# Performance work log

Hardware: AMD Instinct MI355X
Metric: run time of the kernel (lower is better)

## Reference

```python
import jax, jax.numpy as jnp
import numpy as np

# Binary (sign) weight linear: y = x @ sign(W)^T + b

def _binarize(w):
    # sign with sign(0) mapped to +1, as in typical BinaryLinear impls
    return jnp.where(w >= 0, 1.0, -1.0).astype(w.dtype)

def setup_inputs() -> dict:
    key = jax.random.key(0)
    ks = jax.random.split(key, 7)
    B = 65536
    x = jax.random.normal(ks[0], (B, 28, 28), dtype=jnp.float32)
    W1 = jax.random.normal(ks[1], (1000, 784), dtype=jnp.float32) * 0.05
    b1 = jax.random.normal(ks[2], (1000,), dtype=jnp.float32) * 0.01
    W2 = jax.random.normal(ks[3], (500, 1000), dtype=jnp.float32) * 0.05
    b2 = jax.random.normal(ks[4], (500,), dtype=jnp.float32) * 0.01
    W3 = jax.random.normal(ks[5], (10, 500), dtype=jnp.float32) * 0.05
    b3 = jax.random.normal(ks[6], (10,), dtype=jnp.float32) * 0.01
    return {"x": x, "W1": W1, "b1": b1, "W2": W2, "b2": b2, "W3": W3, "b3": b3}

def reference(x, W1, b1, W2, b2, W3, b3):
    h = x.reshape(x.shape[0], -1)                      # [B, 784]
    h = jnp.maximum(h @ _binarize(W1).T + b1, 0.0)     # [B, 1000]
    h = jnp.maximum(h @ _binarize(W2).T + b2, 0.0)     # [B, 500]
    return h @ _binarize(W3).T + b3                    # [B, 10]
```

## Files before the change

kernel.cpp:

```cpp
#include <hip/hip_runtime.h>
#include <stdint.h>


typedef __attribute__((ext_vector_type(8))) short bf16x8;
typedef __attribute__((ext_vector_type(4))) float f32x4;

typedef const __attribute__((address_space(1))) unsigned int* as1_u32p;
typedef __attribute__((address_space(3))) unsigned int* as3_u32p;

__device__ __forceinline__ void glds16(const void* g, void* l) {
  __builtin_amdgcn_global_load_lds((as1_u32p)g, (as3_u32p)l, 16, 0, 0);
}

__device__ __forceinline__ unsigned short f2bf(float f) {
  union { float f; unsigned u; } c;
  c.f = f;
  unsigned u = c.u;
  u += 0x7FFFu + ((u >> 16) & 1u);
  return (unsigned short)(u >> 16);
}

__global__ void binarize_kernel(const float* __restrict__ src, int Ns, int Ks,
                                short* __restrict__ dst, int Np, int Kp) {
  int idx = blockIdx.x * 256 + threadIdx.x;
  if (idx >= Np * Kp) return;
  int n = idx / Kp;
  int k = idx - n * Kp;
  short v = 0;
  if (n < Ns && k < Ks)
    v = (src[n * Ks + k] >= 0.0f) ? (short)0x3F80 : (short)0xBF80;
  dst[idx] = v;
}

__global__ __launch_bounds__(256, 2)
void gemm1_kernel(const float* __restrict__ X, const short* __restrict__ Wb,
                  const float* __restrict__ bias, short* __restrict__ H) {
  constexpr int K = 784, KP = 800, NP = 1024, NR = 1000;
  __shared__ short As[128 * 32];
  __shared__ short Bs[128 * 32];

  const int d = blockIdx.x;
  const int xcd = d & 7;
  const int j = d >> 3;
  const int m0 = ((xcd << 6) + (j >> 3)) * 128;
  const int n0 = (j & 7) * 128;

  const int tid = threadIdx.x;
  const int lane = tid & 63;
  const int wave = tid >> 6;
  const int wm = wave >> 1, wn = wave & 1;
  const int l15 = lane & 15;
  const int quad = lane >> 4;

  const int ar = tid >> 1;
  const int aks = (tid & 1) * 16;
  const float* xrow = X + (size_t)(m0 + ar) * K;
  short* adst = As + ar * 32 + aks;

  const int br = wave * 16 + (lane >> 2);
  const int bks = (lane & 3) * 8;
  const short* brow0 = Wb + (size_t)(n0 + br) * KP + bks;
  short* bdst = Bs + (wave * 16) * 32;

  f32x4 acc[4][4];
#pragma unroll
  for (int i = 0; i < 4; ++i)
#pragma unroll
    for (int j2 = 0; j2 < 4; ++j2) acc[i][j2] = (f32x4){0.f, 0.f, 0.f, 0.f};

  for (int k0 = 0; k0 < KP; k0 += 32) {
    glds16(brow0 + k0, bdst);
    glds16(brow0 + k0 + (size_t)64 * KP, bdst + 64 * 32);
    short tmp[16];
#pragma unroll
    for (int c = 0; c < 4; ++c) {
      const int kk = k0 + aks + c * 4;
      float4 f;
      if (kk < K)
        f = *(const float4*)(xrow + kk);
      else
        f = make_float4(0.f, 0.f, 0.f, 0.f);
      tmp[c * 4 + 0] = (short)f2bf(f.x);
      tmp[c * 4 + 1] = (short)f2bf(f.y);
      tmp[c * 4 + 2] = (short)f2bf(f.z);
      tmp[c * 4 + 3] = (short)f2bf(f.w);
    }
    *(bf16x8*)(adst) = *(bf16x8*)(tmp);
    *(bf16x8*)(adst + 8) = *(bf16x8*)(tmp + 8);

    __syncthreads();

    const short* abase = As + (size_t)(wm * 64 + l15) * 32 + quad * 8;
    const short* bbase = Bs + (size_t)(wn * 64 + l15) * 32 + quad * 8;
    bf16x8 af[4], bfr[4];
#pragma unroll
    for (int i = 0; i < 4; ++i) af[i] = *(const bf16x8*)(abase + i * 16 * 32);
#pragma unroll
    for (int j2 = 0; j2 < 4; ++j2) bfr[j2] = *(const bf16x8*)(bbase + j2 * 16 * 32);
#pragma unroll
    for (int i = 0; i < 4; ++i)
#pragma unroll
      for (int j2 = 0; j2 < 4; ++j2)
        acc[i][j2] = __builtin_amdgcn_mfma_f32_16x16x32_bf16(af[i], bfr[j2], acc[i][j2], 0, 0, 0);
    __syncthreads();
  }

#pragma unroll
  for (int j2 = 0; j2 < 4; ++j2) {
    const int n = n0 + wn * 64 + j2 * 16 + l15;
    const float bv = (n < NR) ? bias[n] : 0.f;
#pragma unroll
    for (int i = 0; i < 4; ++i) {
      const int mr = m0 + wm * 64 + i * 16 + quad * 4;
#pragma unroll
      for (int r = 0; r < 4; ++r) {
        float v = acc[i][j2][r] + bv;
        v = v > 0.f ? v : 0.f;
        H[(size_t)(mr + r) * NP + n] = (short)f2bf(v);
      }
    }
  }
}

template <int KP, int NP, int NR, int GRP, int GRPLOG>
__global__ __launch_bounds__(256, 2)
void gemm_bb(const short* __restrict__ A, const short* __restrict__ Wb,
             const float* __restrict__ bias, short* __restrict__ Hout) {
  __shared__ short As[128 * 32];
  __shared__ short Bs[128 * 32];

  const int d = blockIdx.x;
  const int xcd = d & 7;
  const int j = d >> 3;
  const int m0 = ((xcd << 6) + (j >> GRPLOG)) * 128;
  const int n0 = (j & (GRP - 1)) * 128;

  const int tid = threadIdx.x;
  const int lane = tid & 63;
  const int wave = tid >> 6;
  const int wm = wave >> 1, wn = wave & 1;
  const int l15 = lane & 15;
  const int quad = lane >> 4;

  const int sr = wave * 16 + (lane >> 2);
  const int sks = (lane & 3) * 8;
  const short* asrc = A + (size_t)(m0 + sr) * KP + sks;
  const short* bsrc = Wb + (size_t)(n0 + sr) * KP + sks;
  short* adst = As + (wave * 16) * 32;
  short* bdst = Bs + (wave * 16) * 32;

  f32x4 acc[4][4];
#pragma unroll
  for (int i = 0; i < 4; ++i)
#pragma unroll
    for (int j2 = 0; j2 < 4; ++j2) acc[i][j2] = (f32x4){0.f, 0.f, 0.f, 0.f};

  for (int k0 = 0; k0 < KP; k0 += 32) {
    glds16(asrc + k0, adst);
    glds16(asrc + k0 + (size_t)64 * KP, adst + 64 * 32);
    glds16(bsrc + k0, bdst);
    glds16(bsrc + k0 + (size_t)64 * KP, bdst + 64 * 32);
    __syncthreads();

    const short* abase = As + (size_t)(wm * 64 + l15) * 32 + quad * 8;
    const short* bbase = Bs + (size_t)(wn * 64 + l15) * 32 + quad * 8;
    bf16x8 af[4], bfr[4];
#pragma unroll
    for (int i = 0; i < 4; ++i) af[i] = *(const bf16x8*)(abase + i * 16 * 32);
#pragma unroll
    for (int j2 = 0; j2 < 4; ++j2) bfr[j2] = *(const bf16x8*)(bbase + j2 * 16 * 32);
#pragma unroll
    for (int i = 0; i < 4; ++i)
#pragma unroll
      for (int j2 = 0; j2 < 4; ++j2)
        acc[i][j2] = __builtin_amdgcn_mfma_f32_16x16x32_bf16(af[i], bfr[j2], acc[i][j2], 0, 0, 0);
    __syncthreads();
  }

#pragma unroll
  for (int j2 = 0; j2 < 4; ++j2) {
    const int n = n0 + wn * 64 + j2 * 16 + l15;
    const float bv = (n < NR) ? bias[n] : 0.f;
#pragma unroll
    for (int i = 0; i < 4; ++i) {
      const int mr = m0 + wm * 64 + i * 16 + quad * 4;
#pragma unroll
      for (int r = 0; r < 4; ++r) {
        float v = acc[i][j2][r] + bv;
        v = v > 0.f ? v : 0.f;
        Hout[(size_t)(mr + r) * NP + n] = (short)f2bf(v);
      }
    }
  }
}

__global__ __launch_bounds__(256, 2)
void gemm3_kernel(const short* __restrict__ Hin, const short* __restrict__ Wb,
                  const float* __restrict__ bias, float* __restrict__ Out) {
  constexpr int KP = 512;
  constexpr int BSTRIDE = 520;
  __shared__ short As[128 * 32];
  __shared__ short Bs[16 * BSTRIDE];

  const int tid = threadIdx.x;
  const int lane = tid & 63;
  const int wave = tid >> 6;
  const int l15 = lane & 15;
  const int quad = lane >> 4;
  const int m0 = blockIdx.x * 128;

  for (int t = tid; t < 16 * 512 / 8; t += 256) {
    int n = (t * 8) / 512;
    int k = (t * 8) % 512;
    *(bf16x8*)(Bs + n * BSTRIDE + k) = *(const bf16x8*)(Wb + t * 8);
  }

  const int sr = wave * 16 + (lane >> 2);
  const int sks = (lane & 3) * 8;
  const short* arow0 = Hin + (size_t)(m0 + sr) * KP + sks;
  short* adst = As + (wave * 16) * 32;

  f32x4 acc[2];
#pragma unroll
  for (int i = 0; i < 2; ++i) acc[i] = (f32x4){0.f, 0.f, 0.f, 0.f};

  for (int k0 = 0; k0 < KP; k0 += 32) {
    glds16(arow0 + k0, adst);
    glds16(arow0 + k0 + (size_t)64 * KP, adst + 64 * 32);
    __syncthreads();

    bf16x8 bfr = *(const bf16x8*)(Bs + l15 * BSTRIDE + k0 + quad * 8);
#pragma unroll
    for (int i = 0; i < 2; ++i) {
      bf16x8 af = *(const bf16x8*)(As + (size_t)(wave * 32 + i * 16 + l15) * 32 + quad * 8);
      acc[i] = __builtin_amdgcn_mfma_f32_16x16x32_bf16(af, bfr, acc[i], 0, 0, 0);
    }
    __syncthreads();
  }

  if (l15 < 10) {
    const float bv = bias[l15];
#pragma unroll
    for (int i = 0; i < 2; ++i)
#pragma unroll
      for (int r = 0; r < 4; ++r) {
        const int mr = m0 + wave * 32 + i * 16 + quad * 4 + r;
        Out[(size_t)mr * 10 + l15] = acc[i][r] + bv;
      }
  }
}

extern "C" void kernel_launch(void* const* d_in, const int* in_sizes, int n_in,
                              void* d_out, int out_size, void* d_ws, size_t ws_size,
                              hipStream_t stream) {
  const float* x = (const float*)d_in[0];
  const float* W1 = (const float*)d_in[1];
  const float* b1 = (const float*)d_in[2];
  const float* W2 = (const float*)d_in[3];
  const float* b2 = (const float*)d_in[4];
  const float* W3 = (const float*)d_in[5];
  const float* b3 = (const float*)d_in[6];
  float* out = (float*)d_out;

  uint8_t* p = (uint8_t*)d_ws;
  short* W1b = (short*)p; p += (size_t)1024 * 800 * 2;
  short* W2b = (short*)p; p += (size_t)512 * 1024 * 2;
  short* W3b = (short*)p; p += (size_t)16 * 512 * 2;
  short* h1 = (short*)p; p += (size_t)65536 * 1024 * 2;
  short* h2 = (short*)p;

  binarize_kernel<<<(1024 * 800 + 255) / 256, 256, 0, stream>>>(W1, 1000, 784, W1b, 1024, 800);
  binarize_kernel<<<(512 * 1024 + 255) / 256, 256, 0, stream>>>(W2, 500, 1000, W2b, 512, 1024);
  binarize_kernel<<<(16 * 512 + 255) / 256, 256, 0, stream>>>(W3, 10, 500, W3b, 16, 512);

  gemm1_kernel<<<4096, 256, 0, stream>>>(x, W1b, b1, h1);
  gemm_bb<1024, 512, 500, 4, 2><<<2048, 256, 0, stream>>>(h1, W2b, b2, h2);
  gemm3_kernel<<<512, 256, 0, stream>>>(h2, W3b, b3, out);
}
```

Baseline: 608.4 us.

## Double-buffer gemm1 LDS tiles and restructure gemm3 to load full K at once

Measured after the change: 599.8 us. Within noise of the previous version (-1.4%).

```diff
diff --git a/kernel.cpp b/kernel.cpp
--- a/kernel.cpp
+++ b/kernel.cpp
@@ -36,14 +36,14 @@
 void gemm1_kernel(const float* __restrict__ X, const short* __restrict__ Wb,
                   const float* __restrict__ bias, short* __restrict__ H) {
   constexpr int K = 784, KP = 800, NP = 1024, NR = 1000;
-  __shared__ short As[128 * 32];
-  __shared__ short Bs[128 * 32];
+  __shared__ short As[2][128 * 32];
+  __shared__ short Bs[2][128 * 32];
 
   const int d = blockIdx.x;
   const int xcd = d & 7;
-  const int j = d >> 3;
-  const int m0 = ((xcd << 6) + (j >> 3)) * 128;
-  const int n0 = (j & 7) * 128;
+  const int jj = d >> 3;
+  const int m0 = ((xcd << 6) + (jj >> 3)) * 128;
+  const int n0 = (jj & 7) * 128;
 
   const int tid = threadIdx.x;
   const int lane = tid & 63;
@@ -55,43 +55,59 @@
   const int ar = tid >> 1;
   const int aks = (tid & 1) * 16;
   const float* xrow = X + (size_t)(m0 + ar) * K;
-  short* adst = As + ar * 32 + aks;
 
   const int br = wave * 16 + (lane >> 2);
   const int bks = (lane & 3) * 8;
   const short* brow0 = Wb + (size_t)(n0 + br) * KP + bks;
-  short* bdst = Bs + (wave * 16) * 32;
-
-  f32x4 acc[4][4];
-#pragma unroll
-  for (int i = 0; i < 4; ++i)
-#pragma unroll
-    for (int j2 = 0; j2 < 4; ++j2) acc[i][j2] = (f32x4){0.f, 0.f, 0.f, 0.f};
-
-  for (int k0 = 0; k0 < KP; k0 += 32) {
-    glds16(brow0 + k0, bdst);
-    glds16(brow0 + k0 + (size_t)64 * KP, bdst + 64 * 32);
-    short tmp[16];
+
+  float4 xf[4];
+  auto loadX = [&](int k0) {
 #pragma unroll
     for (int c = 0; c < 4; ++c) {
       const int kk = k0 + aks + c * 4;
-      float4 f;
       if (kk < K)
-        f = *(const float4*)(xrow + kk);
+        xf[c] = *(const float4*)(xrow + kk);
       else
-        f = make_float4(0.f, 0.f, 0.f, 0.f);
-      tmp[c * 4 + 0] = (short)f2bf(f.x);
-      tmp[c * 4 + 1] = (short)f2bf(f.y);
-      tmp[c * 4 + 2] = (short)f2bf(f.z);
-      tmp[c * 4 + 3] = (short)f2bf(f.w);
-    }
-    *(bf16x8*)(adst) = *(bf16x8*)(tmp);
-    *(bf16x8*)(adst + 8) = *(bf16x8*)(tmp + 8);
-
+        xf[c] = make_float4(0.f, 0.f, 0.f, 0.f);
+    }
+  };
+  auto stage = [&](int k0) {
+    const int buf = (k0 >> 5) & 1;
+    short* bd = &Bs[buf][(wave * 16) * 32];
+    glds16(brow0 + k0, bd);
+    glds16(brow0 + k0 + (size_t)64 * KP, bd + 64 * 32);
+    short tmp[16];
+#pragma unroll
+    for (int c = 0; c < 4; ++c) {
+      tmp[c * 4 + 0] = (short)f2bf(xf[c].x);
+      tmp[c * 4 + 1] = (short)f2bf(xf[c].y);
+      tmp[c * 4 + 2] = (short)f2bf(xf[c].z);
+      tmp[c * 4 + 3] = (short)f2bf(xf[c].w);
+    }
+    short* ad = &As[buf][ar * 32 + aks];
+    *(bf16x8*)(ad) = *(bf16x8*)(tmp);
+    *(bf16x8*)(ad + 8) = *(bf16x8*)(tmp + 8);
+  };
+
+  f32x4 acc[4][4];
+#pragma unroll
+  for (int i = 0; i < 4; ++i)
+#pragma unroll
+    for (int j2 = 0; j2 < 4; ++j2) acc[i][j2] = (f32x4){0.f, 0.f, 0.f, 0.f};
+
+  loadX(0);
+  stage(0);
+  loadX(32);
+
+  for (int k0 = 0; k0 < KP; k0 += 32) {
     __syncthreads();
-
-    const short* abase = As + (size_t)(wm * 64 + l15) * 32 + quad * 8;
-    const short* bbase = Bs + (size_t)(wn * 64 + l15) * 32 + quad * 8;
+    if (k0 + 32 < KP) {
+      stage(k0 + 32);
+      if (k0 + 64 < KP) loadX(k0 + 64);
+    }
+    const int buf = (k0 >> 5) & 1;
+    const short* abase = &As[buf][(wm * 64 + l15) * 32 + quad * 8];
+    const short* bbase = &Bs[buf][(wn * 64 + l15) * 32 + quad * 8];
     bf16x8 af[4], bfr[4];
 #pragma unroll
     for (int i = 0; i < 4; ++i) af[i] = *(const bf16x8*)(abase + i * 16 * 32);
@@ -102,7 +118,6 @@
 #pragma unroll
       for (int j2 = 0; j2 < 4; ++j2)
         acc[i][j2] = __builtin_amdgcn_mfma_f32_16x16x32_bf16(af[i], bfr[j2], acc[i][j2], 0, 0, 0);
-    __syncthreads();
   }
 
 #pragma unroll
@@ -198,55 +213,43 @@
 void gemm3_kernel(const short* __restrict__ Hin, const short* __restrict__ Wb,
                   const float* __restrict__ bias, float* __restrict__ Out) {
   constexpr int KP = 512;
-  constexpr int BSTRIDE = 520;
-  __shared__ short As[128 * 32];
-  __shared__ short Bs[16 * BSTRIDE];
+  __shared__ short As[64 * KP];
 
   const int tid = threadIdx.x;
   const int lane = tid & 63;
   const int wave = tid >> 6;
   const int l15 = lane & 15;
   const int quad = lane >> 4;
-  const int m0 = blockIdx.x * 128;
-
-  for (int t = tid; t < 16 * 512 / 8; t += 256) {
-    int n = (t * 8) / 512;
-    int k = (t * 8) % 512;
-    *(bf16x8*)(Bs + n * BSTRIDE + k) = *(const bf16x8*)(Wb + t * 8);
-  }
-
-  const int sr = wave * 16 + (lane >> 2);
-  const int sks = (lane & 3) * 8;
-  const short* arow0 = Hin + (size_t)(m0 + sr) * KP + sks;
-  short* adst = As + (wave * 16) * 32;
-
-  f32x4 acc[2];
-#pragma unroll
-  for (int i = 0; i < 2; ++i) acc[i] = (f32x4){0.f, 0.f, 0.f, 0.f};
-
-  for (int k0 = 0; k0 < KP; k0 += 32) {
-    glds16(arow0 + k0, adst);
-    glds16(arow0 + k0 + (size_t)64 * KP, adst + 64 * 32);
-    __syncthreads();
-
-    bf16x8 bfr = *(const bf16x8*)(Bs + l15 * BSTRIDE + k0 + quad * 8);
-#pragma unroll
-    for (int i = 0; i < 2; ++i) {
-      bf16x8 af = *(const bf16x8*)(As + (size_t)(wave * 32 + i * 16 + l15) * 32 + quad * 8);
-      acc[i] = __builtin_amdgcn_mfma_f32_16x16x32_bf16(af, bfr, acc[i], 0, 0, 0);
-    }
-    __syncthreads();
+  const int m0 = blockIdx.x * 64;
+
+  bf16x8 bw[16];
+#pragma unroll
+  for (int kk = 0; kk < 16; ++kk)
+    bw[kk] = *(const bf16x8*)(Wb + l15 * KP + kk * 32 + quad * 8);
+
+  const short* asrc = Hin + (size_t)(m0 + wave * 16) * KP + lane * 8;
+  short* adst = As + (size_t)(wave * 16) * KP;
+#pragma unroll
+  for (int t = 0; t < 16; ++t)
+    glds16(asrc + (size_t)t * KP, adst + (size_t)t * KP);
+
+  __syncthreads();
+
+  f32x4 acc = (f32x4){0.f, 0.f, 0.f, 0.f};
+  const short* abase = As + (size_t)(wave * 16 + l15) * KP + quad * 8;
+#pragma unroll
+  for (int kk = 0; kk < 16; ++kk) {
+    bf16x8 af = *(const bf16x8*)(abase + kk * 32);
+    acc = __builtin_amdgcn_mfma_f32_16x16x32_bf16(af, bw[kk], acc, 0, 0, 0);
   }
 
   if (l15 < 10) {
     const float bv = bias[l15];
 #pragma unroll
-    for (int i = 0; i < 2; ++i)
-#pragma unroll
-      for (int r = 0; r < 4; ++r) {
-        const int mr = m0 + wave * 32 + i * 16 + quad * 4 + r;
-        Out[(size_t)mr * 10 + l15] = acc[i][r] + bv;
-      }
+    for (int r = 0; r < 4; ++r) {
+      const int mr = m0 + wave * 16 + quad * 4 + r;
+      Out[(size_t)mr * 10 + l15] = acc[r] + bv;
+    }
   }
 }
 
@@ -275,5 +278,5 @@
 
   gemm1_kernel<<<4096, 256, 0, stream>>>(x, W1b, b1, h1);
   gemm_bb<1024, 512, 500, 4, 2><<<2048, 256, 0, stream>>>(h1, W2b, b2, h2);
-  gemm3_kernel<<<512, 256, 0, stream>>>(h2, W3b, b3, out);
-}
+  gemm3_kernel<<<1024, 256, 0, stream>>>(h2, W3b, b3, out);
+}
```
